# Kernel tuning notes

Measured on AMD Instinct MI355X. Metric: run time of the kernel, lower is better.

Reference implementation:

```python
import jax, jax.numpy as jnp
import numpy as np


def setup_inputs() -> dict:
    key = jax.random.key(0)
    ks = jax.random.split(key, 5)
    B, C, D, H, W = 2, 256, 8, 28, 28
    mid = C // 2
    # Kaiming-normal-ish init (std = sqrt(2/fan_in)) for 1x1 conv weights
    def kaiming(k, shape, fan_in):
        return jax.random.normal(k, shape, dtype=jnp.float32) * np.sqrt(2.0 / fan_in)
    x = jax.random.normal(ks[0], (B, C, D, H, W), dtype=jnp.float32)
    w1 = kaiming(ks[1], (mid, C), C)
    w2 = kaiming(ks[2], (mid, C), C)
    w3 = kaiming(ks[3], (mid, C), C)
    w4 = kaiming(ks[4], (C, mid), mid)
    b1 = jnp.zeros((mid,), jnp.float32)
    b2 = jnp.zeros((mid,), jnp.float32)
    b3 = jnp.zeros((mid,), jnp.float32)
    b4 = jnp.zeros((C,), jnp.float32)
    return {"x": x, "w1": w1, "b1": b1, "w2": w2, "b2": b2,
            "w3": w3, "b3": b3, "w4": w4, "b4": b4}


def reference(x, w1, b1, w2, b2, w3, b3, w4, b4):
    # x: [B, C, D, H, W]; 1x1x1 Conv3d == channel matmul over flattened N = D*H*W
    B, C, D, H, W = x.shape
    N = D * H * W
    xf = x.reshape(B, C, N)                                   # [B, C, N]
    # theta: conv1 -> [B, N, mid]
    e1 = jnp.einsum('mc,bcn->bnm', w1, xf) + b1               # [B, N, mid]
    # phi: conv2 -> [B, mid, N]
    e2 = jnp.einsum('mc,bcn->bmn', w2, xf) + b2[:, None]      # [B, mid, N]
    # g: conv3 -> [B, N, mid]
    e3 = jnp.einsum('mc,bcn->bnm', w3, xf) + b3               # [B, N, mid]
    # unscaled attention: softmax over keys (last axis)
    kernel = jnp.einsum('bnm,bmk->bnk', e1, e2)               # [B, N, N]
    kernel = jax.nn.softmax(kernel, axis=2)
    attn = jnp.einsum('bnk,bkm->bnm', kernel, e3)             # [B, N, mid]
    # conv4 (1x1 Conv1d): mid -> C, applied on [B, mid, N]
    y = jnp.einsum('cm,bnm->bcn', w4, attn) + b4[:, None]     # [B, C, N]
    return x + y.reshape(B, C, D, H, W)
```

## Files before the change

kernel.cpp:

```cpp
#include <hip/hip_runtime.h>


#define BB  2
#define CC  256
#define NN  6272
#define MID 128
#define KSPLIT 4

typedef _Float16 half4_t __attribute__((ext_vector_type(4)));
typedef _Float16 half8_t __attribute__((ext_vector_type(8)));
typedef float    floatx16 __attribute__((ext_vector_type(16)));

__device__ __forceinline__ void fma4(float4& a, const float4 v, const float s) {
    a.x += v.x * s; a.y += v.y * s; a.z += v.z * s; a.w += v.w * s;
}
__device__ __forceinline__ float dot4(const float4 a, const float4 b) {
    return a.x * b.x + a.y * b.y + a.z * b.z + a.w * b.w;
}

__global__ __launch_bounds__(256, 2) void proj_kernel(
    const float* __restrict__ x,
    const float* __restrict__ w1, const float* __restrict__ bi1,
    const float* __restrict__ w2, const float* __restrict__ bi2,
    const float* __restrict__ w3, const float* __restrict__ bi3,
    _Float16* __restrict__ Qg, _Float16* __restrict__ Kg, _Float16* __restrict__ VtG)
{
    const int t  = threadIdx.x;
    const int n0 = blockIdx.x * 64;
    const int pj = blockIdx.y;
    const int b  = blockIdx.z;
    const float* w  = (pj == 0) ? w1 : (pj == 1) ? w2 : w3;
    const float* bi = (pj == 0) ? bi1 : (pj == 1) ? bi2 : bi3;

    __shared__ float xs[CC * 68];
    {
        const float* xb = x + (size_t)b * CC * NN;
        for (int r = t; r < CC * 16; r += 256) {
            int c = r >> 4, j = (r & 15) << 2;
            float4 v = *(const float4*)(xb + (size_t)c * NN + n0 + j);
            *(float4*)&xs[c * 68 + j] = v;
        }
    }
    __syncthreads();

    const int n4 = (t & 15) << 2;
    const int m0 = (t >> 4) << 3;
    float4 acc4[8];
    #pragma unroll
    for (int k = 0; k < 8; ++k) acc4[k] = make_float4(0.f, 0.f, 0.f, 0.f);

    for (int cc = 0; cc < CC; cc += 4) {
        float4 xv[4];
        #pragma unroll
        for (int u = 0; u < 4; ++u)
            xv[u] = *(const float4*)&xs[(cc + u) * 68 + n4];
        #pragma unroll
        for (int k = 0; k < 8; ++k) {
            float4 wq = *(const float4*)(w + (size_t)(m0 + k) * CC + cc);
            fma4(acc4[k], xv[0], wq.x);
            fma4(acc4[k], xv[1], wq.y);
            fma4(acc4[k], xv[2], wq.z);
            fma4(acc4[k], xv[3], wq.w);
        }
    }

    const float* af = (const float*)acc4;
    float bb[8];
    #pragma unroll
    for (int k = 0; k < 8; ++k) bb[k] = bi[m0 + k];

    if (pj < 2) {
        _Float16* eo = ((pj == 0) ? Qg : Kg) + (size_t)b * NN * MID;
        #pragma unroll
        for (int i = 0; i < 4; ++i) {
            half8_t h;
            #pragma unroll
            for (int k = 0; k < 8; ++k) h[k] = (_Float16)(af[k * 4 + i] + bb[k]);
            *(half8_t*)(eo + (size_t)(n0 + n4 + i) * MID + m0) = h;
        }
    } else {
        _Float16* eo = VtG + (size_t)b * MID * NN;
        #pragma unroll
        for (int k = 0; k < 8; ++k) {
            half4_t h;
            #pragma unroll
            for (int i = 0; i < 4; ++i) h[i] = (_Float16)(af[k * 4 + i] + bb[k]);
            *(half4_t*)(eo + (size_t)(m0 + k) * NN + n0 + n4) = h;
        }
    }
}

__global__ __launch_bounds__(256, 3) void attn_kernel(
    const _Float16* __restrict__ Qg, const _Float16* __restrict__ Kg,
    const _Float16* __restrict__ VtG, _Float16* __restrict__ Opart,
    float* __restrict__ Mst, float* __restrict__ Lst)
{
    const int t    = threadIdx.x;
    const int lane = t & 63;
    const int wave = t >> 6;
    const int qh   = wave & 1;
    const int kh   = wave >> 1;
    const int l31  = lane & 31;
    const int l5   = lane >> 5;
    const int q0   = blockIdx.x * 64;
    const int split= blockIdx.y;
    const int b    = blockIdx.z;

    const int t0   = split * 24 + (split < 2 ? split : 2);
    const int tcnt = (split < 2) ? 25 : 24;

    __shared__ __align__(16) char lds[46208];
    _Float16* Ks = (_Float16*)lds;
    _Float16* Vt = (_Float16*)(lds + 17408);
    _Float16* Pt = (_Float16*)(lds + 35840);
    float* msh   = (float*)(lds + 45056);
    float* lsh   = msh + 144;
    float* Obuf  = (float*)lds;

    const _Float16* Qb = Qg + ((size_t)b * NN + q0 + qh * 32) * MID;
    const _Float16* Kb = Kg + (size_t)b * NN * MID;
    const _Float16* Vb = VtG + (size_t)b * MID * NN;

    half8_t qf[8];
    #pragma unroll
    for (int ds = 0; ds < 8; ++ds)
        qf[ds] = *(const half8_t*)(Qb + (size_t)l31 * MID + ds * 16 + l5 * 8);

    floatx16 o[4];
    #pragma unroll
    for (int dt = 0; dt < 4; ++dt)
        #pragma unroll
        for (int j = 0; j < 16; ++j) o[dt][j] = 0.f;
    float m_run = -3.0e38f, l_run = 0.f;

    for (int kt = t0; kt < t0 + tcnt; ++kt) {
        const int nk = kt * 64;
        #pragma unroll
        for (int it = 0; it < 4; ++it) {
            int c = it * 256 + t;
            int r = c >> 4, off = (c & 15) * 8;
            *(half8_t*)(Ks + r * 136 + off) =
                *(const half8_t*)(Kb + (size_t)(nk + r) * MID + off);
        }
        #pragma unroll
        for (int it = 0; it < 4; ++it) {
            int c = it * 256 + t;
            int d = c >> 3, off = (c & 7) * 8;
            *(half8_t*)(Vt + d * 72 + off) =
                *(const half8_t*)(Vb + (size_t)d * NN + nk + off);
        }
        __syncthreads();

        floatx16 s;
        #pragma unroll
        for (int j = 0; j < 16; ++j) s[j] = 0.f;
        const _Float16* krow = Ks + (kh * 32 + l31) * 136 + l5 * 8;
        #pragma unroll
        for (int ds = 0; ds < 8; ++ds)
            s = __builtin_amdgcn_mfma_f32_32x32x16_f16(
                    *(const half8_t*)(krow + ds * 16), qf[ds], s, 0, 0, 0);

        float tmax = s[0];
        #pragma unroll
        for (int j = 1; j < 16; ++j) tmax = fmaxf(tmax, s[j]);
        tmax = fmaxf(tmax, __shfl_xor(tmax, 32));
        const float m_new = fmaxf(m_run, tmax);
        const float alpha = __expf(m_run - m_new);
        m_run = m_new;

        float psum = 0.f;
        _Float16* prow = Pt + (qh * 32 + l31) * 72 + kh * 32 + 4 * l5;
        #pragma unroll
        for (int g = 0; g < 4; ++g) {
            float p0 = __expf(s[4 * g + 0] - m_new);
            float p1 = __expf(s[4 * g + 1] - m_new);
            float p2 = __expf(s[4 * g + 2] - m_new);
            float p3 = __expf(s[4 * g + 3] - m_new);
            psum += (p0 + p1) + (p2 + p3);
            half4_t h;
            h[0] = (_Float16)p0; h[1] = (_Float16)p1;
            h[2] = (_Float16)p2; h[3] = (_Float16)p3;
            *(half4_t*)(prow + 8 * g) = h;
        }
        psum += __shfl_xor(psum, 32);
        l_run = l_run * alpha + psum;

        #pragma unroll
        for (int dt = 0; dt < 4; ++dt)
            #pragma unroll
            for (int j = 0; j < 16; ++j) o[dt][j] *= alpha;

        __builtin_amdgcn_s_waitcnt(0xC07F);

        #pragma unroll
        for (int ks = 0; ks < 2; ++ks) {
            half8_t pf = *(const half8_t*)(Pt + (qh * 32 + l31) * 72 +
                                           kh * 32 + ks * 16 + l5 * 8);
            const _Float16* vcol = Vt + kh * 32 + ks * 16 + l5 * 8;
            #pragma unroll
            for (int dt = 0; dt < 4; ++dt)
                o[dt] = __builtin_amdgcn_mfma_f32_32x32x16_f16(
                            *(const half8_t*)(vcol + (dt * 32 + l31) * 72), pf,
                            o[dt], 0, 0, 0);
        }
        __syncthreads();
    }

    const int qm = qh * 32 + l31;
    if (l5 == 0) { msh[kh * 72 + qm] = m_run; lsh[kh * 72 + qm] = l_run; }
    __syncthreads();
    const float m0v = msh[qm], m1v = msh[72 + qm];
    const float M   = fmaxf(m0v, m1v);
    const float Lt  = lsh[qm] * __expf(m0v - M) + lsh[72 + qm] * __expf(m1v - M);
    const float sc  = __expf(m_run - M) / Lt;

    if (kh == 0) {
        #pragma unroll
        for (int dt = 0; dt < 4; ++dt)
            #pragma unroll
            for (int j = 0; j < 16; ++j) {
                int d = dt * 32 + (j & 3) + 8 * (j >> 2) + 4 * l5;
                Obuf[qm * 132 + d] = o[dt][j] * sc;
            }
    }
    __syncthreads();
    if (kh == 1) {
        #pragma unroll
        for (int dt = 0; dt < 4; ++dt)
            #pragma unroll
            for (int j = 0; j < 16; ++j) {
                int d = dt * 32 + (j & 3) + 8 * (j >> 2) + 4 * l5;
                Obuf[qm * 132 + d] += o[dt][j] * sc;
            }
    }
    __syncthreads();

    _Float16* Ob = Opart + ((size_t)(b * KSPLIT + split) * NN + q0) * MID;
    #pragma unroll
    for (int it = 0; it < 4; ++it) {
        int c = it * 256 + t;
        int q = c >> 4, off = (c & 15) * 8;
        half8_t h;
        #pragma unroll
        for (int j = 0; j < 8; ++j) h[j] = (_Float16)Obuf[q * 132 + off + j];
        *(half8_t*)(Ob + (size_t)q * MID + off) = h;
    }
    if (t < 64) {
        const float a0 = msh[t], a1 = msh[72 + t];
        const float MM = fmaxf(a0, a1);
        const float LL = lsh[t] * __expf(a0 - MM) + lsh[72 + t] * __expf(a1 - MM);
        const size_t idx = (size_t)(b * KSPLIT + split) * NN + q0 + t;
        Mst[idx] = MM;
        Lst[idx] = LL;
    }
}

__global__ __launch_bounds__(256, 2) void epi_kernel(
    const _Float16* __restrict__ Opart, const float* __restrict__ Mst,
    const float* __restrict__ Lst, const float* __restrict__ w4,
    const float* __restrict__ b4, const float* __restrict__ x,
    float* __restrict__ out)
{
    const int t  = threadIdx.x;
    const int n0 = blockIdx.x * 32;
    const int ch = blockIdx.y;
    const int b  = blockIdx.z;

    __shared__ float as[32 * 132];
    __shared__ float wts[KSPLIT][36];

    if (t < 32) {
        float m[KSPLIT], l[KSPLIT];
        #pragma unroll
        for (int s = 0; s < KSPLIT; ++s) {
            const size_t idx = (size_t)(b * KSPLIT + s) * NN + n0 + t;
            m[s] = Mst[idx]; l[s] = Lst[idx];
        }
        float M = m[0];
        #pragma unroll
        for (int s = 1; s < KSPLIT; ++s) M = fmaxf(M, m[s]);
        float L = 0.f, wl[KSPLIT];
        #pragma unroll
        for (int s = 0; s < KSPLIT; ++s) { wl[s] = l[s] * __expf(m[s] - M); L += wl[s]; }
        const float inv = 1.0f / L;
        #pragma unroll
        for (int s = 0; s < KSPLIT; ++s) wts[s][t] = wl[s] * inv;
    }
    __syncthreads();

    for (int r = t; r < 32 * 16; r += 256) {
        int q = r >> 4, off = (r & 15) * 8;
        float acc[8];
        #pragma unroll
        for (int j = 0; j < 8; ++j) acc[j] = 0.f;
        #pragma unroll
        for (int s = 0; s < KSPLIT; ++s) {
            const float wv = wts[s][q];
            half8_t h = *(const half8_t*)(Opart +
                ((size_t)(b * KSPLIT + s) * NN + n0 + q) * MID + off);
            #pragma unroll
            for (int j = 0; j < 8; ++j) acc[j] += wv * (float)h[j];
        }
        *(float4*)&as[q * 132 + off]     = make_float4(acc[0], acc[1], acc[2], acc[3]);
        *(float4*)&as[q * 132 + off + 4] = make_float4(acc[4], acc[5], acc[6], acc[7]);
    }
    __syncthreads();

    const int n4 = (t & 7) << 2;
    const int c0 = ch * 128 + (t >> 3) * 4;
    float4 accE[4];
    #pragma unroll
    for (int k = 0; k < 4; ++k) accE[k] = make_float4(0.f, 0.f, 0.f, 0.f);

    for (int ms = 0; ms < 32; ++ms) {
        float4 av[4];
        #pragma unroll
        for (int i = 0; i < 4; ++i)
            av[i] = *(const float4*)&as[(n4 + i) * 132 + (ms << 2)];
        #pragma unroll
        for (int k = 0; k < 4; ++k) {
            float4 wq = *(const float4*)(w4 + (size_t)(c0 + k) * MID + (ms << 2));
            accE[k].x += dot4(av[0], wq);
            accE[k].y += dot4(av[1], wq);
            accE[k].z += dot4(av[2], wq);
            accE[k].w += dot4(av[3], wq);
        }
    }

    #pragma unroll
    for (int k = 0; k < 4; ++k) {
        const int c = c0 + k;
        const float bv = b4[c];
        const size_t off = ((size_t)b * CC + c) * NN + n0 + n4;
        float4 xr = *(const float4*)(x + off);
        float4 r;
        r.x = accE[k].x + bv + xr.x;
        r.y = accE[k].y + bv + xr.y;
        r.z = accE[k].z + bv + xr.z;
        r.w = accE[k].w + bv + xr.w;
        *(float4*)(out + off) = r;
    }
}

extern "C" void kernel_launch(void* const* d_in, const int* in_sizes, int n_in,
                              void* d_out, int out_size, void* d_ws, size_t ws_size,
                              hipStream_t stream)
{
    const float* x  = (const float*)d_in[0];
    const float* w1 = (const float*)d_in[1];
    const float* b1 = (const float*)d_in[2];
    const float* w2 = (const float*)d_in[3];
    const float* b2 = (const float*)d_in[4];
    const float* w3 = (const float*)d_in[5];
    const float* b3 = (const float*)d_in[6];
    const float* w4 = (const float*)d_in[7];
    const float* b4 = (const float*)d_in[8];
    float* out = (float*)d_out;

    _Float16* Qg    = (_Float16*)d_ws;
    _Float16* Kg    = Qg + (size_t)BB * NN * MID;
    _Float16* VtG   = Kg + (size_t)BB * NN * MID;
    _Float16* Opart = VtG + (size_t)BB * NN * MID;
    float*    Mst   = (float*)(Opart + (size_t)BB * KSPLIT * NN * MID);
    float*    Lst   = Mst + (size_t)BB * KSPLIT * NN;

    proj_kernel<<<dim3(NN / 64, 3, BB), 256, 0, stream>>>(x, w1, b1, w2, b2, w3, b3, Qg, Kg, VtG);
    attn_kernel<<<dim3(NN / 64, KSPLIT, BB), 256, 0, stream>>>(Qg, Kg, VtG, Opart, Mst, Lst);
    epi_kernel<<<dim3(NN / 32, 2, BB), 256, 0, stream>>>(Opart, Mst, Lst, w4, b4, x, out);
}
```

Before: 311.5 us.

## Restructure attention to per-wave direct-load K/V and retile projection/epilogue

The attention kernel drops the shared-memory K/V staging and the block-wide barriers. Each wave now loads its K and V fragments straight from global memory into registers and works on 32-key steps, while the two wave pairs split the key range between them. Blocks are mapped to XCDs by split and batch, and the softmax rescale is skipped when no lane's max increases. The projection and epilogue kernels move to smaller tiles with higher occupancy bounds, and the V transpose write goes through LDS for coalescing. The cost is less K/V reuse through LDS, which means more global or L2 traffic per wave.

```diff
diff --git a/kernel.cpp b/kernel.cpp
--- a/kernel.cpp
+++ b/kernel.cpp
@@ -18,7 +18,7 @@
     return a.x * b.x + a.y * b.y + a.z * b.z + a.w * b.w;
 }
 
-__global__ __launch_bounds__(256, 2) void proj_kernel(
+__global__ __launch_bounds__(256, 4) void proj_kernel(
     const float* __restrict__ x,
     const float* __restrict__ w1, const float* __restrict__ bi1,
     const float* __restrict__ w2, const float* __restrict__ bi2,
@@ -26,66 +26,74 @@
     _Float16* __restrict__ Qg, _Float16* __restrict__ Kg, _Float16* __restrict__ VtG)
 {
     const int t  = threadIdx.x;
-    const int n0 = blockIdx.x * 64;
+    const int n0 = blockIdx.x * 32;
     const int pj = blockIdx.y;
     const int b  = blockIdx.z;
     const float* w  = (pj == 0) ? w1 : (pj == 1) ? w2 : w3;
     const float* bi = (pj == 0) ? bi1 : (pj == 1) ? bi2 : bi3;
 
-    __shared__ float xs[CC * 68];
+    __shared__ float xs[CC * 36];
+    _Float16* es = (_Float16*)xs;
+
     {
         const float* xb = x + (size_t)b * CC * NN;
-        for (int r = t; r < CC * 16; r += 256) {
-            int c = r >> 4, j = (r & 15) << 2;
-            float4 v = *(const float4*)(xb + (size_t)c * NN + n0 + j);
-            *(float4*)&xs[c * 68 + j] = v;
-        }
-    }
-    __syncthreads();
-
-    const int n4 = (t & 15) << 2;
-    const int m0 = (t >> 4) << 3;
-    float4 acc4[8];
-    #pragma unroll
-    for (int k = 0; k < 8; ++k) acc4[k] = make_float4(0.f, 0.f, 0.f, 0.f);
+        for (int r = t; r < CC * 8; r += 256) {
+            int c = r >> 3, j = (r & 7) << 2;
+            *(float4*)&xs[c * 36 + j] = *(const float4*)(xb + (size_t)c * NN + n0 + j);
+        }
+    }
+    __syncthreads();
+
+    const int n4 = (t & 7) << 2;
+    const int m0 = (t >> 3) << 2;
+    float4 acc[4];
+    #pragma unroll
+    for (int k = 0; k < 4; ++k) acc[k] = make_float4(0.f, 0.f, 0.f, 0.f);
 
     for (int cc = 0; cc < CC; cc += 4) {
         float4 xv[4];
         #pragma unroll
         for (int u = 0; u < 4; ++u)
-            xv[u] = *(const float4*)&xs[(cc + u) * 68 + n4];
-        #pragma unroll
-        for (int k = 0; k < 8; ++k) {
+            xv[u] = *(const float4*)&xs[(cc + u) * 36 + n4];
+        #pragma unroll
+        for (int k = 0; k < 4; ++k) {
             float4 wq = *(const float4*)(w + (size_t)(m0 + k) * CC + cc);
-            fma4(acc4[k], xv[0], wq.x);
-            fma4(acc4[k], xv[1], wq.y);
-            fma4(acc4[k], xv[2], wq.z);
-            fma4(acc4[k], xv[3], wq.w);
-        }
-    }
-
-    const float* af = (const float*)acc4;
-    float bb[8];
-    #pragma unroll
-    for (int k = 0; k < 8; ++k) bb[k] = bi[m0 + k];
+            fma4(acc[k], xv[0], wq.x);
+            fma4(acc[k], xv[1], wq.y);
+            fma4(acc[k], xv[2], wq.z);
+            fma4(acc[k], xv[3], wq.w);
+        }
+    }
+
+    const float* af = (const float*)acc;
+    float bv[4];
+    #pragma unroll
+    for (int k = 0; k < 4; ++k) bv[k] = bi[m0 + k];
 
     if (pj < 2) {
         _Float16* eo = ((pj == 0) ? Qg : Kg) + (size_t)b * NN * MID;
         #pragma unroll
         for (int i = 0; i < 4; ++i) {
-            half8_t h;
-            #pragma unroll
-            for (int k = 0; k < 8; ++k) h[k] = (_Float16)(af[k * 4 + i] + bb[k]);
-            *(half8_t*)(eo + (size_t)(n0 + n4 + i) * MID + m0) = h;
+            half4_t h;
+            #pragma unroll
+            for (int k = 0; k < 4; ++k) h[k] = (_Float16)(af[k * 4 + i] + bv[k]);
+            *(half4_t*)(eo + (size_t)(n0 + n4 + i) * MID + m0) = h;
         }
     } else {
+        __syncthreads();
+        #pragma unroll
+        for (int k = 0; k < 4; ++k)
+            #pragma unroll
+            for (int i = 0; i < 4; ++i)
+                es[(m0 + k) * 36 + n4 + i] = (_Float16)(af[k * 4 + i] + bv[k]);
+        __syncthreads();
         _Float16* eo = VtG + (size_t)b * MID * NN;
-        #pragma unroll
-        for (int k = 0; k < 8; ++k) {
-            half4_t h;
-            #pragma unroll
-            for (int i = 0; i < 4; ++i) h[i] = (_Float16)(af[k * 4 + i] + bb[k]);
-            *(half4_t*)(eo + (size_t)(m0 + k) * NN + n0 + n4) = h;
+        const int j4 = (t & 7) << 2;
+        #pragma unroll
+        for (int it = 0; it < 4; ++it) {
+            int d = it * 32 + (t >> 3);
+            *(half4_t*)(eo + (size_t)d * NN + n0 + j4) =
+                *(const half4_t*)&es[d * 36 + j4];
         }
     }
 }
@@ -99,23 +107,26 @@
     const int lane = t & 63;
     const int wave = t >> 6;
     const int qh   = wave & 1;
-    const int kh   = wave >> 1;
+    const int kseg = wave >> 1;
     const int l31  = lane & 31;
     const int l5   = lane >> 5;
-    const int q0   = blockIdx.x * 64;
-    const int split= blockIdx.y;
-    const int b    = blockIdx.z;
-
-    const int t0   = split * 24 + (split < 2 ? split : 2);
-    const int tcnt = (split < 2) ? 25 : 24;
-
-    __shared__ __align__(16) char lds[46208];
-    _Float16* Ks = (_Float16*)lds;
-    _Float16* Vt = (_Float16*)(lds + 17408);
-    _Float16* Pt = (_Float16*)(lds + 35840);
-    float* msh   = (float*)(lds + 45056);
-    float* lsh   = msh + 144;
-    float* Obuf  = (float*)lds;
+
+    const int g     = blockIdx.x;
+    const int xcd   = g & 7;
+    const int split = xcd & 3;
+    const int b     = xcd >> 2;
+    const int q0    = (g >> 3) * 64;
+
+    const int step0  = split * 49 + (kseg ? 25 : 0);
+    const int nsteps = kseg ? 24 : 25;
+
+    __shared__ __align__(16) char lds[35072];
+    _Float16* PtB = (_Float16*)lds;
+    float* Obuf   = (float*)lds;
+    float* msh    = (float*)(lds + 33792);
+    float* lsh    = msh + 144;
+
+    _Float16* Ptw = PtB + wave * (32 * 36);
 
     const _Float16* Qb = Qg + ((size_t)b * NN + q0 + qh * 32) * MID;
     const _Float16* Kb = Kg + (size_t)b * NN * MID;
@@ -133,88 +144,88 @@
         for (int j = 0; j < 16; ++j) o[dt][j] = 0.f;
     float m_run = -3.0e38f, l_run = 0.f;
 
-    for (int kt = t0; kt < t0 + tcnt; ++kt) {
-        const int nk = kt * 64;
-        #pragma unroll
-        for (int it = 0; it < 4; ++it) {
-            int c = it * 256 + t;
-            int r = c >> 4, off = (c & 15) * 8;
-            *(half8_t*)(Ks + r * 136 + off) =
-                *(const half8_t*)(Kb + (size_t)(nk + r) * MID + off);
-        }
-        #pragma unroll
-        for (int it = 0; it < 4; ++it) {
-            int c = it * 256 + t;
-            int d = c >> 3, off = (c & 7) * 8;
-            *(half8_t*)(Vt + d * 72 + off) =
-                *(const half8_t*)(Vb + (size_t)d * NN + nk + off);
-        }
-        __syncthreads();
+    const _Float16* kp0 = Kb + (size_t)l31 * MID + l5 * 8;
+    const _Float16* vp0 = Vb + (size_t)l31 * NN + l5 * 8;
+
+    for (int st = 0; st < nsteps; ++st) {
+        const int nk = (step0 + st) * 32;
+
+        const _Float16* kp = kp0 + (size_t)nk * MID;
+        half8_t kf[8];
+        #pragma unroll
+        for (int ds = 0; ds < 8; ++ds)
+            kf[ds] = *(const half8_t*)(kp + ds * 16);
 
         floatx16 s;
         #pragma unroll
         for (int j = 0; j < 16; ++j) s[j] = 0.f;
-        const _Float16* krow = Ks + (kh * 32 + l31) * 136 + l5 * 8;
         #pragma unroll
         for (int ds = 0; ds < 8; ++ds)
-            s = __builtin_amdgcn_mfma_f32_32x32x16_f16(
-                    *(const half8_t*)(krow + ds * 16), qf[ds], s, 0, 0, 0);
+            s = __builtin_amdgcn_mfma_f32_32x32x16_f16(kf[ds], qf[ds], s, 0, 0, 0);
+
+        const _Float16* vp = vp0 + nk;
+        half8_t vf[8];
+        #pragma unroll
+        for (int dt = 0; dt < 4; ++dt)
+            #pragma unroll
+            for (int ks = 0; ks < 2; ++ks)
+                vf[dt * 2 + ks] = *(const half8_t*)(vp + (size_t)(dt * 32) * NN + ks * 16);
 
         float tmax = s[0];
         #pragma unroll
         for (int j = 1; j < 16; ++j) tmax = fmaxf(tmax, s[j]);
         tmax = fmaxf(tmax, __shfl_xor(tmax, 32));
-        const float m_new = fmaxf(m_run, tmax);
-        const float alpha = __expf(m_run - m_new);
-        m_run = m_new;
+
+        float m_new = m_run;
+        if (__any(tmax > m_run)) {
+            m_new = fmaxf(m_run, tmax);
+            const float alpha = __expf(m_run - m_new);
+            l_run *= alpha;
+            #pragma unroll
+            for (int dt = 0; dt < 4; ++dt)
+                #pragma unroll
+                for (int j = 0; j < 16; ++j) o[dt][j] *= alpha;
+            m_run = m_new;
+        }
 
         float psum = 0.f;
-        _Float16* prow = Pt + (qh * 32 + l31) * 72 + kh * 32 + 4 * l5;
-        #pragma unroll
-        for (int g = 0; g < 4; ++g) {
-            float p0 = __expf(s[4 * g + 0] - m_new);
-            float p1 = __expf(s[4 * g + 1] - m_new);
-            float p2 = __expf(s[4 * g + 2] - m_new);
-            float p3 = __expf(s[4 * g + 3] - m_new);
+        _Float16* prow = Ptw + l31 * 36 + 4 * l5;
+        #pragma unroll
+        for (int gg = 0; gg < 4; ++gg) {
+            float p0 = __expf(s[4 * gg + 0] - m_new);
+            float p1 = __expf(s[4 * gg + 1] - m_new);
+            float p2 = __expf(s[4 * gg + 2] - m_new);
+            float p3 = __expf(s[4 * gg + 3] - m_new);
             psum += (p0 + p1) + (p2 + p3);
             half4_t h;
             h[0] = (_Float16)p0; h[1] = (_Float16)p1;
             h[2] = (_Float16)p2; h[3] = (_Float16)p3;
-            *(half4_t*)(prow + 8 * g) = h;
+            *(half4_t*)(prow + 8 * gg) = h;
         }
         psum += __shfl_xor(psum, 32);
-        l_run = l_run * alpha + psum;
-
-        #pragma unroll
-        for (int dt = 0; dt < 4; ++dt)
-            #pragma unroll
-            for (int j = 0; j < 16; ++j) o[dt][j] *= alpha;
+        l_run += psum;
 
         __builtin_amdgcn_s_waitcnt(0xC07F);
 
         #pragma unroll
         for (int ks = 0; ks < 2; ++ks) {
-            half8_t pf = *(const half8_t*)(Pt + (qh * 32 + l31) * 72 +
-                                           kh * 32 + ks * 16 + l5 * 8);
-            const _Float16* vcol = Vt + kh * 32 + ks * 16 + l5 * 8;
+            half8_t pf = *(const half8_t*)(Ptw + l31 * 36 + ks * 16 + l5 * 8);
             #pragma unroll
             for (int dt = 0; dt < 4; ++dt)
                 o[dt] = __builtin_amdgcn_mfma_f32_32x32x16_f16(
-                            *(const half8_t*)(vcol + (dt * 32 + l31) * 72), pf,
-                            o[dt], 0, 0, 0);
-        }
-        __syncthreads();
+                            vf[dt * 2 + ks], pf, o[dt], 0, 0, 0);
+        }
     }
 
     const int qm = qh * 32 + l31;
-    if (l5 == 0) { msh[kh * 72 + qm] = m_run; lsh[kh * 72 + qm] = l_run; }
+    if (l5 == 0) { msh[kseg * 72 + qm] = m_run; lsh[kseg * 72 + qm] = l_run; }
     __syncthreads();
     const float m0v = msh[qm], m1v = msh[72 + qm];
     const float M   = fmaxf(m0v, m1v);
     const float Lt  = lsh[qm] * __expf(m0v - M) + lsh[72 + qm] * __expf(m1v - M);
     const float sc  = __expf(m_run - M) / Lt;
 
-    if (kh == 0) {
+    if (kseg == 0) {
         #pragma unroll
         for (int dt = 0; dt < 4; ++dt)
             #pragma unroll
@@ -224,7 +235,7 @@
             }
     }
     __syncthreads();
-    if (kh == 1) {
+    if (kseg == 1) {
         #pragma unroll
         for (int dt = 0; dt < 4; ++dt)
             #pragma unroll
@@ -255,7 +266,7 @@
     }
 }
 
-__global__ __launch_bounds__(256, 2) void epi_kernel(
+__global__ __launch_bounds__(256, 4) void epi_kernel(
     const _Float16* __restrict__ Opart, const float* __restrict__ Mst,
     const float* __restrict__ Lst, const float* __restrict__ w4,
     const float* __restrict__ b4, const float* __restrict__ x,
@@ -307,10 +318,10 @@
     __syncthreads();
 
     const int n4 = (t & 7) << 2;
-    const int c0 = ch * 128 + (t >> 3) * 4;
-    float4 accE[4];
-    #pragma unroll
-    for (int k = 0; k < 4; ++k) accE[k] = make_float4(0.f, 0.f, 0.f, 0.f);
+    const int c0 = ch * 64 + (t >> 3) * 2;
+    float4 accE[2];
+    #pragma unroll
+    for (int k = 0; k < 2; ++k) accE[k] = make_float4(0.f, 0.f, 0.f, 0.f);
 
     for (int ms = 0; ms < 32; ++ms) {
         float4 av[4];
@@ -318,7 +329,7 @@
         for (int i = 0; i < 4; ++i)
             av[i] = *(const float4*)&as[(n4 + i) * 132 + (ms << 2)];
         #pragma unroll
-        for (int k = 0; k < 4; ++k) {
+        for (int k = 0; k < 2; ++k) {
             float4 wq = *(const float4*)(w4 + (size_t)(c0 + k) * MID + (ms << 2));
             accE[k].x += dot4(av[0], wq);
             accE[k].y += dot4(av[1], wq);
@@ -328,16 +339,16 @@
     }
 
     #pragma unroll
-    for (int k = 0; k < 4; ++k) {
+    for (int k = 0; k < 2; ++k) {
         const int c = c0 + k;
-        const float bv = b4[c];
+        const float bvv = b4[c];
         const size_t off = ((size_t)b * CC + c) * NN + n0 + n4;
         float4 xr = *(const float4*)(x + off);
         float4 r;
-        r.x = accE[k].x + bv + xr.x;
-        r.y = accE[k].y + bv + xr.y;
-        r.z = accE[k].z + bv + xr.z;
-        r.w = accE[k].w + bv + xr.w;
+        r.x = accE[k].x + bvv + xr.x;
+        r.y = accE[k].y + bvv + xr.y;
+        r.z = accE[k].z + bvv + xr.z;
+        r.w = accE[k].w + bvv + xr.w;
         *(float4*)(out + off) = r;
     }
 }
@@ -364,7 +375,7 @@
     float*    Mst   = (float*)(Opart + (size_t)BB * KSPLIT * NN * MID);
     float*    Lst   = Mst + (size_t)BB * KSPLIT * NN;
 
-    proj_kernel<<<dim3(NN / 64, 3, BB), 256, 0, stream>>>(x, w1, b1, w2, b2, w3, b3, Qg, Kg, VtG);
-    attn_kernel<<<dim3(NN / 64, KSPLIT, BB), 256, 0, stream>>>(Qg, Kg, VtG, Opart, Mst, Lst);
-    epi_kernel<<<dim3(NN / 32, 2, BB), 256, 0, stream>>>(Opart, Mst, Lst, w4, b4, x, out);
-}
+    proj_kernel<<<dim3(NN / 32, 3, BB), 256, 0, stream>>>(x, w1, b1, w2, b2, w3, b3, Qg, Kg, VtG);
+    attn_kernel<<<dim3(98 * 8), 256, 0, stream>>>(Qg, Kg, VtG, Opart, Mst, Lst);
+    epi_kernel<<<dim3(NN / 32, 4, BB), 256, 0, stream>>>(Opart, Mst, Lst, w4, b4, x, out);
+}
```

Result: slower. 331.4 us (+6.4%).
